# Performance work log

Measured on AMD Instinct MI355X. Metric: run time of the kernel, lower is better.

## Reference

```python
import jax, jax.numpy as jnp
import numpy as np


def setup_inputs() -> dict:
    key = jax.random.key(0)
    k0, k1, k2, k3 = jax.random.split(key, 4)
    T, H, I, E = 2048, 2048, 5632, 8
    return {
        "hidden_states": jax.random.normal(k0, (T, H), dtype=jnp.float32),
        "gate_w": jax.random.normal(k1, (E, H), dtype=jnp.float32) * 0.02,
        "w1": jax.random.normal(k2, (E, 2 * I, H), dtype=jnp.float32) * 0.02,
        "w2": jax.random.normal(k3, (E, H, I), dtype=jnp.float32) * 0.02,
        "top_k": 2,
    }


def reference(hidden_states, gate_w, w1, w2, top_k):
    # hidden_states: [T, H]; gate_w: [E, H]; w1: [E, 2I, H]; w2: [E, H, I]
    T = hidden_states.shape[0]
    E = w1.shape[0]
    router_logits = hidden_states @ gate_w.T                    # [T, E]
    probs = jax.nn.softmax(router_logits, axis=-1)
    topk_w, topk_idx = jax.lax.top_k(probs, top_k)              # [T, k]
    # renormalize=False in fused_moe: use raw softmax top-k weights.
    # Dense combine matrix C[t, e] = weight of expert e for token t (0 if unrouted).
    combine = jnp.zeros((T, E), dtype=probs.dtype)
    combine = combine.at[jnp.arange(T)[:, None], topk_idx].add(topk_w)
    out = jnp.zeros_like(hidden_states)
    for e in range(E):  # small fixed expert loop
        gate_up = hidden_states @ w1[e].T                       # [T, 2I]
        g, u = jnp.split(gate_up, 2, axis=-1)
        h = jax.nn.silu(g) * u                                  # SiluAndMul
        out = out + combine[:, e:e + 1] * (h @ w2[e].T)         # [T, H]
    return out
```

## Files before the change

kernel.cpp:

```cpp
#include <hip/hip_runtime.h>
#include <hip/hip_bf16.h>

typedef __bf16 bf16_t;
typedef __bf16 bf16x4 __attribute__((ext_vector_type(4)));
typedef __bf16 bf16x8 __attribute__((ext_vector_type(8)));
typedef float  f32x4  __attribute__((ext_vector_type(4)));

constexpr int T_ = 2048, H_ = 2048, I_ = 5632, E_ = 8, S_ = T_ * 2;

constexpr size_t OFF_HB    = 0;
constexpr size_t OFF_HOUT  = OFF_HB    + (size_t)T_ * H_ * 2;
constexpr size_t OFF_DPART = OFF_HOUT  + (size_t)S_ * I_ * 2;
constexpr size_t OFF_TOS   = OFF_DPART + (size_t)S_ * H_ * 4;
constexpr size_t OFF_SOT   = OFF_TOS   + (size_t)S_ * 4;
constexpr size_t OFF_TKI   = OFF_SOT   + (size_t)S_ * 4;
constexpr size_t OFF_TKW   = OFF_TKI   + (size_t)S_ * 4;
constexpr size_t OFF_CNT   = OFF_TKW   + (size_t)S_ * 4;
constexpr size_t OFF_OFFS  = OFF_CNT   + 64;
constexpr size_t OFF_CUR   = OFF_OFFS  + 64;

__device__ __forceinline__ void gload16(const void* g, void* l) {
  __builtin_amdgcn_global_load_lds(
      (const __attribute__((address_space(1))) void*)g,
      (__attribute__((address_space(3))) void*)l, 16, 0, 0);
}

__device__ __forceinline__ bf16x4 cvt4(const float4 v) {
  bf16x4 r; r[0]=(bf16_t)v.x; r[1]=(bf16_t)v.y; r[2]=(bf16_t)v.z; r[3]=(bf16_t)v.w;
  return r;
}

__global__ __launch_bounds__(256)
void router_kernel(const float* __restrict__ hs, const float* __restrict__ gw,
                   int* __restrict__ tki, float* __restrict__ tkw,
                   int* __restrict__ counts, bf16_t* __restrict__ hb)
{
  const int t = blockIdx.x;
  const int tid = threadIdx.x;
  const int lane = tid & 63, wid = tid >> 6;
  const float* hrow = hs + (size_t)t * H_;
  const int c0 = tid * 8;
  float4 h0 = *(const float4*)(hrow + c0);
  float4 h1 = *(const float4*)(hrow + c0 + 4);
  bf16x8 hv;
  hv[0]=(bf16_t)h0.x; hv[1]=(bf16_t)h0.y; hv[2]=(bf16_t)h0.z; hv[3]=(bf16_t)h0.w;
  hv[4]=(bf16_t)h1.x; hv[5]=(bf16_t)h1.y; hv[6]=(bf16_t)h1.z; hv[7]=(bf16_t)h1.w;
  *(bf16x8*)(hb + (size_t)t * H_ + c0) = hv;

  float acc[E_];
  #pragma unroll
  for (int e = 0; e < E_; ++e) {
    const float* g = gw + (size_t)e * H_ + c0;
    float4 g0 = *(const float4*)(g);
    float4 g1 = *(const float4*)(g + 4);
    acc[e] = h0.x*g0.x + h0.y*g0.y + h0.z*g0.z + h0.w*g0.w
           + h1.x*g1.x + h1.y*g1.y + h1.z*g1.z + h1.w*g1.w;
  }
  #pragma unroll
  for (int e = 0; e < E_; ++e)
    #pragma unroll
    for (int o = 32; o > 0; o >>= 1)
      acc[e] += __shfl_down(acc[e], o);
  __shared__ float red[4][E_];
  if (lane == 0)
    #pragma unroll
    for (int e = 0; e < E_; ++e) red[wid][e] = acc[e];
  __syncthreads();
  if (tid == 0) {
    float l[E_];
    #pragma unroll
    for (int e = 0; e < E_; ++e) l[e] = red[0][e] + red[1][e] + red[2][e] + red[3][e];
    float m = l[0];
    #pragma unroll
    for (int e = 1; e < E_; ++e) m = fmaxf(m, l[e]);
    float p[E_]; float s = 0.f;
    #pragma unroll
    for (int e = 0; e < E_; ++e) { p[e] = __expf(l[e] - m); s += p[e]; }
    int i1 = 0;
    #pragma unroll
    for (int e = 1; e < E_; ++e) if (l[e] > l[i1]) i1 = e;
    int i2 = (i1 == 0) ? 1 : 0;
    #pragma unroll
    for (int e = 0; e < E_; ++e) if (e != i1 && l[e] > l[i2]) i2 = e;
    tki[2*t] = i1; tki[2*t+1] = i2;
    tkw[2*t] = p[i1] / s; tkw[2*t+1] = p[i2] / s;
    atomicAdd(&counts[i1], 1);
    atomicAdd(&counts[i2], 1);
  }
}

__global__ void scan_kernel(const int* __restrict__ counts, const int* __restrict__ tki,
                            int* __restrict__ offs, int* __restrict__ cursor,
                            int* __restrict__ tos, int* __restrict__ sot)
{
  if (threadIdx.x == 0) {
    int run = 0;
    for (int e = 0; e < E_; ++e) { offs[e] = run; cursor[e] = run; run += counts[e]; }
  }
  __syncthreads();
  for (int t = threadIdx.x; t < T_; t += blockDim.x) {
    #pragma unroll
    for (int k = 0; k < 2; ++k) {
      int e = tki[2*t + k];
      int s = atomicAdd(&cursor[e], 1);
      tos[s] = t;
      sot[2*t + k] = s;
    }
  }
}

constexpr int G1_BM = 128, G1_BN = 64, G1_BK = 64;

__global__ __launch_bounds__(256, 2)
void gemm1_kernel(const bf16_t* __restrict__ hb, const float* __restrict__ w1,
                  const int* __restrict__ tos, const int* __restrict__ offs,
                  const int* __restrict__ counts, bf16_t* __restrict__ hout)
{
  const int bid = blockIdx.x;
  const int e   = bid & 7;
  const int idx = bid >> 3;
  const int mt  = idx & 15;
  const int nt  = idx >> 4;

  const int cnt = counts[e];
  const int m0 = mt * G1_BM;
  if (m0 >= cnt) return;
  const int off = offs[e];
  const int n0 = nt * G1_BN;

  const float* Wg = w1 + (size_t)e * (2 * (size_t)I_ * H_) + (size_t)n0 * H_;
  const float* Wu = Wg + (size_t)I_ * H_;

  __shared__ bf16_t Al [2][G1_BM][G1_BK];
  __shared__ bf16_t Bgl[2][G1_BN][G1_BK];
  __shared__ bf16_t Bul[2][G1_BN][G1_BK];

  const int tid = threadIdx.x;
  const int lane = tid & 63, wid = tid >> 6;
  const int wm = wid >> 1, wn = wid & 1;
  const int l15 = lane & 15, l4 = lane >> 4;

  const bf16_t* agp[4]; int aoff[4];
  #pragma unroll
  for (int i = 0; i < 4; ++i) {
    int q = wid * 4 + i;
    int row = q * 8 + (lane >> 3);
    int slot = off + m0 + row, mx = off + cnt - 1;
    if (slot > mx) slot = mx;
    agp[i]  = hb + (size_t)tos[slot] * H_ + ((lane & 7) ^ (lane >> 3)) * 8;
    aoff[i] = q * 1024;
  }
  const int brow = tid >> 2, bq = tid & 3;
  const float* gsrc = Wg + (size_t)brow * H_;
  const float* usrc = Wu + (size_t)brow * H_;
  int wby[4];
  #pragma unroll
  for (int i = 0; i < 4; ++i)
    wby[i] = brow * 128 + ((8 * bq + 32 * i) ^ ((brow & 7) << 4));

  float4 bgr[4], bur[4];
  auto loadB = [&](int k0) {
    #pragma unroll
    for (int i = 0; i < 4; ++i) bgr[i] = *(const float4*)(gsrc + k0 + 4 * bq + 16 * i);
    #pragma unroll
    for (int i = 0; i < 4; ++i) bur[i] = *(const float4*)(usrc + k0 + 4 * bq + 16 * i);
  };
  auto stageA = [&](int b, int k0) {
    char* base = (char*)&Al[b][0][0];
    #pragma unroll
    for (int i = 0; i < 4; ++i) gload16(agp[i] + k0, base + aoff[i]);
  };
  auto writeB = [&](int b) {
    char* gb = (char*)&Bgl[b][0][0];
    char* ub = (char*)&Bul[b][0][0];
    #pragma unroll
    for (int i = 0; i < 4; ++i) {
      *(bf16x4*)(gb + wby[i]) = cvt4(bgr[i]);
      *(bf16x4*)(ub + wby[i]) = cvt4(bur[i]);
    }
  };

  f32x4 accg[4][2], accu[4][2];
  #pragma unroll
  for (int mi = 0; mi < 4; ++mi)
    #pragma unroll
    for (int ni = 0; ni < 2; ++ni) {
      accg[mi][ni] = f32x4{0.f,0.f,0.f,0.f};
      accu[mi][ni] = f32x4{0.f,0.f,0.f,0.f};
    }

  auto compute = [&](int b) {
    const char* ab = (const char*)&Al[b][0][0];
    const char* gb = (const char*)&Bgl[b][0][0];
    const char* ub = (const char*)&Bul[b][0][0];
    #pragma unroll
    for (int ks = 0; ks < 2; ++ks) {
      const int cb = ks * 64 + l4 * 16;
      bf16x8 af[4], bgf[2], buf2[2];
      #pragma unroll
      for (int mi = 0; mi < 4; ++mi) {
        int r = wm * 64 + mi * 16 + l15;
        af[mi] = *(const bf16x8*)(ab + r * 128 + (cb ^ ((r & 7) << 4)));
      }
      #pragma unroll
      for (int ni = 0; ni < 2; ++ni) {
        int r = wn * 32 + ni * 16 + l15;
        int o = r * 128 + (cb ^ ((r & 7) << 4));
        bgf[ni]  = *(const bf16x8*)(gb + o);
        buf2[ni] = *(const bf16x8*)(ub + o);
      }
      #pragma unroll
      for (int mi = 0; mi < 4; ++mi)
        #pragma unroll
        for (int ni = 0; ni < 2; ++ni) {
          accg[mi][ni] = __builtin_amdgcn_mfma_f32_16x16x32_bf16(af[mi], bgf[ni],  accg[mi][ni], 0, 0, 0);
          accu[mi][ni] = __builtin_amdgcn_mfma_f32_16x16x32_bf16(af[mi], buf2[ni], accu[mi][ni], 0, 0, 0);
        }
    }
  };

  constexpr int NK = H_ / G1_BK;
  stageA(0, 0); loadB(0); writeB(0);
  __syncthreads();
  int cur = 0;
  for (int kt = 0; kt < NK; ++kt) {
    if (kt + 1 < NK) { stageA(cur ^ 1, (kt + 1) * G1_BK); loadB((kt + 1) * G1_BK); }
    compute(cur);
    if (kt + 1 < NK) writeB(cur ^ 1);
    __syncthreads();
    cur ^= 1;
  }

  #pragma unroll
  for (int mi = 0; mi < 4; ++mi)
    #pragma unroll
    for (int ni = 0; ni < 2; ++ni)
      #pragma unroll
      for (int j = 0; j < 4; ++j) {
        int rel = wm*64 + mi*16 + l4*4 + j;
        if (m0 + rel < cnt) {
          int col = n0 + wn*32 + ni*16 + l15;
          float g = accg[mi][ni][j];
          float u = accu[mi][ni][j];
          float hvv = (g / (1.0f + __expf(-g))) * u;
          hout[(size_t)(off + m0 + rel) * I_ + col] = (bf16_t)hvv;
        }
      }
}

constexpr int G2_BM = 128, G2_BN = 128, G2_BK = 64;

__global__ __launch_bounds__(256, 2)
void gemm2_kernel(const bf16_t* __restrict__ hbuf, const float* __restrict__ w2,
                  const int* __restrict__ offs, const int* __restrict__ counts,
                  float* __restrict__ dpart)
{
  const int bid = blockIdx.x;
  const int e   = bid & 7;
  const int idx = bid >> 3;
  const int mt  = idx & 15;
  const int nt  = idx >> 4;

  const int cnt = counts[e];
  const int m0 = mt * G2_BM;
  if (m0 >= cnt) return;
  const int off = offs[e];
  const int n0 = nt * G2_BN;
  const float* W = w2 + (size_t)e * ((size_t)H_ * I_) + (size_t)n0 * I_;

  __shared__ bf16_t Al[2][G2_BM][G2_BK];
  __shared__ bf16_t Bl[2][G2_BN][G2_BK];

  const int tid = threadIdx.x;
  const int lane = tid & 63, wid = tid >> 6;
  const int wm = wid >> 1, wn = wid & 1;
  const int l15 = lane & 15, l4 = lane >> 4;

  const bf16_t* agp[4]; int aoff[4];
  #pragma unroll
  for (int i = 0; i < 4; ++i) {
    int q = wid * 4 + i;
    int row = q * 8 + (lane >> 3);
    int slot = off + m0 + row, mx = off + cnt - 1;
    if (slot > mx) slot = mx;
    agp[i]  = hbuf + (size_t)slot * I_ + ((lane & 7) ^ (lane >> 3)) * 8;
    aoff[i] = q * 1024;
  }
  const int brow = tid >> 1, bq = tid & 1;
  const float* bsrc = W + (size_t)brow * I_;
  int wby[8];
  #pragma unroll
  for (int i = 0; i < 8; ++i)
    wby[i] = brow * 128 + ((8 * bq + 16 * i) ^ ((brow & 7) << 4));

  float4 br[8];
  auto loadB = [&](int k0) {
    #pragma unroll
    for (int i = 0; i < 8; ++i) br[i] = *(const float4*)(bsrc + k0 + 4 * bq + 8 * i);
  };
  auto stageA = [&](int b, int k0) {
    char* base = (char*)&Al[b][0][0];
    #pragma unroll
    for (int i = 0; i < 4; ++i) gload16(agp[i] + k0, base + aoff[i]);
  };
  auto writeB = [&](int b) {
    char* bb = (char*)&Bl[b][0][0];
    #pragma unroll
    for (int i = 0; i < 8; ++i)
      *(bf16x4*)(bb + wby[i]) = cvt4(br[i]);
  };

  f32x4 acc[4][4];
  #pragma unroll
  for (int mi = 0; mi < 4; ++mi)
    #pragma unroll
    for (int ni = 0; ni < 4; ++ni) acc[mi][ni] = f32x4{0.f,0.f,0.f,0.f};

  auto compute = [&](int b) {
    const char* ab = (const char*)&Al[b][0][0];
    const char* bb = (const char*)&Bl[b][0][0];
    #pragma unroll
    for (int ks = 0; ks < 2; ++ks) {
      const int cb = ks * 64 + l4 * 16;
      bf16x8 af[4], bf[4];
      #pragma unroll
      for (int mi = 0; mi < 4; ++mi) {
        int r = wm * 64 + mi * 16 + l15;
        af[mi] = *(const bf16x8*)(ab + r * 128 + (cb ^ ((r & 7) << 4)));
      }
      #pragma unroll
      for (int ni = 0; ni < 4; ++ni) {
        int r = wn * 64 + ni * 16 + l15;
        bf[ni] = *(const bf16x8*)(bb + r * 128 + (cb ^ ((r & 7) << 4)));
      }
      #pragma unroll
      for (int mi = 0; mi < 4; ++mi)
        #pragma unroll
        for (int ni = 0; ni < 4; ++ni)
          acc[mi][ni] = __builtin_amdgcn_mfma_f32_16x16x32_bf16(af[mi], bf[ni], acc[mi][ni], 0, 0, 0);
    }
  };

  constexpr int NK = I_ / G2_BK;
  stageA(0, 0); loadB(0); writeB(0);
  __syncthreads();
  int cur = 0;
  for (int kt = 0; kt < NK; ++kt) {
    if (kt + 1 < NK) { stageA(cur ^ 1, (kt + 1) * G2_BK); loadB((kt + 1) * G2_BK); }
    compute(cur);
    if (kt + 1 < NK) writeB(cur ^ 1);
    __syncthreads();
    cur ^= 1;
  }

  #pragma unroll
  for (int mi = 0; mi < 4; ++mi)
    #pragma unroll
    for (int ni = 0; ni < 4; ++ni)
      #pragma unroll
      for (int j = 0; j < 4; ++j) {
        int rel = wm*64 + mi*16 + l4*4 + j;
        if (m0 + rel < cnt) {
          int col = n0 + wn*64 + ni*16 + l15;
          dpart[(size_t)(off + m0 + rel) * H_ + col] = acc[mi][ni][j];
        }
      }
}

__global__ __launch_bounds__(256)
void combine_kernel(const float* __restrict__ dpart, const int* __restrict__ sot,
                    const float* __restrict__ tkw, float* __restrict__ out)
{
  int idx = blockIdx.x * 256 + threadIdx.x;
  int t = idx >> 9;
  int c = (idx & 511) * 4;
  float wA = tkw[2*t], wB = tkw[2*t+1];
  int sA = sot[2*t], sB = sot[2*t+1];
  float4 a = *(const float4*)(dpart + (size_t)sA * H_ + c);
  float4 b = *(const float4*)(dpart + (size_t)sB * H_ + c);
  float4 o;
  o.x = wA*a.x + wB*b.x; o.y = wA*a.y + wB*b.y;
  o.z = wA*a.z + wB*b.z; o.w = wA*a.w + wB*b.w;
  *(float4*)(out + (size_t)t * H_ + c) = o;
}

extern "C" void kernel_launch(void* const* d_in, const int* in_sizes, int n_in,
                              void* d_out, int out_size, void* d_ws, size_t ws_size,
                              hipStream_t stream) {
  const float* hs = (const float*)d_in[0];
  const float* gw = (const float*)d_in[1];
  const float* w1 = (const float*)d_in[2];
  const float* w2 = (const float*)d_in[3];
  float* out = (float*)d_out;
  char* ws = (char*)d_ws;

  bf16_t* hb    = (bf16_t*)(ws + OFF_HB);
  bf16_t* hout  = (bf16_t*)(ws + OFF_HOUT);
  float*  dpart = (float*) (ws + OFF_DPART);
  int*    tos   = (int*)   (ws + OFF_TOS);
  int*    sot   = (int*)   (ws + OFF_SOT);
  int*    tki   = (int*)   (ws + OFF_TKI);
  float*  tkw   = (float*) (ws + OFF_TKW);
  int*    cnt   = (int*)   (ws + OFF_CNT);
  int*    offp  = (int*)   (ws + OFF_OFFS);
  int*    curp  = (int*)   (ws + OFF_CUR);

  hipMemsetAsync(ws + OFF_CNT, 0, 64, stream);

  router_kernel<<<T_, 256, 0, stream>>>(hs, gw, tki, tkw, cnt, hb);
  scan_kernel<<<1, 256, 0, stream>>>(cnt, tki, offp, curp, tos, sot);
  gemm1_kernel<<<(T_ / G1_BM) * (I_ / G1_BN) * E_, 256, 0, stream>>>(hb, w1, tos, offp, cnt, hout);
  gemm2_kernel<<<(T_ / G2_BM) * (H_ / G2_BN) * E_, 256, 0, stream>>>(hout, w2, offp, cnt, dpart);
  combine_kernel<<<(T_ * H_ / 4) / 256, 256, 0, stream>>>(dpart, sot, tkw, out);
}
```

Measured before the change: 1.033 ms.

## Stage fp32 expert weights directly into LDS via async loads, convert at fragment read

Both expert GEMMs now load the fp32 weight tiles straight into shared memory with global_load_lds, the same way the activations were already loaded. The register staging and the separate bf16 write-back step are gone, and the conversion to bf16 happens when each wave reads its MFMA fragments. This removes register pressure and the in-loop writeB stall, and lets the weight fetch overlap compute asynchronously. To fit the larger fp32 LDS tiles, BK is halved to 32 and the occupancy hint is raised to 3. The barrier also moves to the top of the loop. The trade-offs are redundant conversion across waves, more LDS read bandwidth, and twice as many k-iterations and barriers.

```diff
diff --git a/kernel.cpp b/kernel.cpp
--- a/kernel.cpp
+++ b/kernel.cpp
@@ -2,7 +2,6 @@
 #include <hip/hip_bf16.h>
 
 typedef __bf16 bf16_t;
-typedef __bf16 bf16x4 __attribute__((ext_vector_type(4)));
 typedef __bf16 bf16x8 __attribute__((ext_vector_type(8)));
 typedef float  f32x4  __attribute__((ext_vector_type(4)));
 
@@ -23,11 +22,6 @@
   __builtin_amdgcn_global_load_lds(
       (const __attribute__((address_space(1))) void*)g,
       (__attribute__((address_space(3))) void*)l, 16, 0, 0);
-}
-
-__device__ __forceinline__ bf16x4 cvt4(const float4 v) {
-  bf16x4 r; r[0]=(bf16_t)v.x; r[1]=(bf16_t)v.y; r[2]=(bf16_t)v.z; r[3]=(bf16_t)v.w;
-  return r;
 }
 
 __global__ __launch_bounds__(256)
@@ -109,9 +103,9 @@
   }
 }
 
-constexpr int G1_BM = 128, G1_BN = 64, G1_BK = 64;
-
-__global__ __launch_bounds__(256, 2)
+constexpr int G1_BM = 128, G1_BN = 64, G1_BK = 32;
+
+__global__ __launch_bounds__(256, 3)
 void gemm1_kernel(const bf16_t* __restrict__ hb, const float* __restrict__ w1,
                   const int* __restrict__ tos, const int* __restrict__ offs,
                   const int* __restrict__ counts, bf16_t* __restrict__ hout)
@@ -132,52 +126,45 @@
   const float* Wu = Wg + (size_t)I_ * H_;
 
   __shared__ bf16_t Al [2][G1_BM][G1_BK];
-  __shared__ bf16_t Bgl[2][G1_BN][G1_BK];
-  __shared__ bf16_t Bul[2][G1_BN][G1_BK];
+  __shared__ float  Bgl[2][G1_BN][G1_BK];
+  __shared__ float  Bul[2][G1_BN][G1_BK];
 
   const int tid = threadIdx.x;
   const int lane = tid & 63, wid = tid >> 6;
   const int wm = wid >> 1, wn = wid & 1;
   const int l15 = lane & 15, l4 = lane >> 4;
 
-  const bf16_t* agp[4]; int aoff[4];
-  #pragma unroll
-  for (int i = 0; i < 4; ++i) {
-    int q = wid * 4 + i;
-    int row = q * 8 + (lane >> 3);
+  const bf16_t* agp[2]; int aoff[2];
+  #pragma unroll
+  for (int i = 0; i < 2; ++i) {
+    int q = wid * 2 + i;
+    int row = q * 16 + (lane >> 2);
     int slot = off + m0 + row, mx = off + cnt - 1;
     if (slot > mx) slot = mx;
-    agp[i]  = hb + (size_t)tos[slot] * H_ + ((lane & 7) ^ (lane >> 3)) * 8;
+    agp[i]  = hb + (size_t)tos[slot] * H_ + (lane & 3) * 8;
     aoff[i] = q * 1024;
   }
-  const int brow = tid >> 2, bq = tid & 3;
-  const float* gsrc = Wg + (size_t)brow * H_;
-  const float* usrc = Wu + (size_t)brow * H_;
-  int wby[4];
-  #pragma unroll
-  for (int i = 0; i < 4; ++i)
-    wby[i] = brow * 128 + ((8 * bq + 32 * i) ^ ((brow & 7) << 4));
-
-  float4 bgr[4], bur[4];
-  auto loadB = [&](int k0) {
-    #pragma unroll
-    for (int i = 0; i < 4; ++i) bgr[i] = *(const float4*)(gsrc + k0 + 4 * bq + 16 * i);
-    #pragma unroll
-    for (int i = 0; i < 4; ++i) bur[i] = *(const float4*)(usrc + k0 + 4 * bq + 16 * i);
-  };
-  auto stageA = [&](int b, int k0) {
-    char* base = (char*)&Al[b][0][0];
-    #pragma unroll
-    for (int i = 0; i < 4; ++i) gload16(agp[i] + k0, base + aoff[i]);
-  };
-  auto writeB = [&](int b) {
+  const float* bgp[2]; const float* bup[2]; int boff[2];
+  #pragma unroll
+  for (int i = 0; i < 2; ++i) {
+    int q = wid * 2 + i;
+    int row = q * 8 + (lane >> 3);
+    int scol = ((lane & 7) ^ (lane >> 3)) * 4;
+    bgp[i]  = Wg + (size_t)row * H_ + scol;
+    bup[i]  = Wu + (size_t)row * H_ + scol;
+    boff[i] = q * 1024;
+  }
+
+  auto stage = [&](int b, int k0) {
+    char* ab = (char*)&Al [b][0][0];
     char* gb = (char*)&Bgl[b][0][0];
     char* ub = (char*)&Bul[b][0][0];
     #pragma unroll
-    for (int i = 0; i < 4; ++i) {
-      *(bf16x4*)(gb + wby[i]) = cvt4(bgr[i]);
-      *(bf16x4*)(ub + wby[i]) = cvt4(bur[i]);
-    }
+    for (int i = 0; i < 2; ++i) gload16(agp[i] + k0, ab + aoff[i]);
+    #pragma unroll
+    for (int i = 0; i < 2; ++i) gload16(bgp[i] + k0, gb + boff[i]);
+    #pragma unroll
+    for (int i = 0; i < 2; ++i) gload16(bup[i] + k0, ub + boff[i]);
   };
 
   f32x4 accg[4][2], accu[4][2];
@@ -190,44 +177,50 @@
     }
 
   auto compute = [&](int b) {
-    const char* ab = (const char*)&Al[b][0][0];
+    const char* ab = (const char*)&Al [b][0][0];
     const char* gb = (const char*)&Bgl[b][0][0];
     const char* ub = (const char*)&Bul[b][0][0];
-    #pragma unroll
-    for (int ks = 0; ks < 2; ++ks) {
-      const int cb = ks * 64 + l4 * 16;
-      bf16x8 af[4], bgf[2], buf2[2];
-      #pragma unroll
-      for (int mi = 0; mi < 4; ++mi) {
-        int r = wm * 64 + mi * 16 + l15;
-        af[mi] = *(const bf16x8*)(ab + r * 128 + (cb ^ ((r & 7) << 4)));
+    bf16x8 af[4], bgf[2], buf2[2];
+    #pragma unroll
+    for (int mi = 0; mi < 4; ++mi) {
+      int r = wm * 64 + mi * 16 + l15;
+      af[mi] = *(const bf16x8*)(ab + r * 64 + l4 * 16);
+    }
+    #pragma unroll
+    for (int ni = 0; ni < 2; ++ni) {
+      int r = wn * 32 + ni * 16 + l15;
+      const char* rbg = gb + r * 128;
+      const char* rbu = ub + r * 128;
+      int c0 = (l4 * 32)      ^ ((r & 7) << 4);
+      int c1 = (l4 * 32 + 16) ^ ((r & 7) << 4);
+      f32x4 g0 = *(const f32x4*)(rbg + c0);
+      f32x4 g1 = *(const f32x4*)(rbg + c1);
+      f32x4 u0 = *(const f32x4*)(rbu + c0);
+      f32x4 u1 = *(const f32x4*)(rbu + c1);
+      #pragma unroll
+      for (int j = 0; j < 4; ++j) {
+        bgf[ni][j]     = (bf16_t)g0[j];
+        bgf[ni][j + 4] = (bf16_t)g1[j];
+        buf2[ni][j]     = (bf16_t)u0[j];
+        buf2[ni][j + 4] = (bf16_t)u1[j];
       }
+    }
+    #pragma unroll
+    for (int mi = 0; mi < 4; ++mi)
       #pragma unroll
       for (int ni = 0; ni < 2; ++ni) {
-        int r = wn * 32 + ni * 16 + l15;
-        int o = r * 128 + (cb ^ ((r & 7) << 4));
-        bgf[ni]  = *(const bf16x8*)(gb + o);
-        buf2[ni] = *(const bf16x8*)(ub + o);
+        accg[mi][ni] = __builtin_amdgcn_mfma_f32_16x16x32_bf16(af[mi], bgf[ni],  accg[mi][ni], 0, 0, 0);
+        accu[mi][ni] = __builtin_amdgcn_mfma_f32_16x16x32_bf16(af[mi], buf2[ni], accu[mi][ni], 0, 0, 0);
       }
-      #pragma unroll
-      for (int mi = 0; mi < 4; ++mi)
-        #pragma unroll
-        for (int ni = 0; ni < 2; ++ni) {
-          accg[mi][ni] = __builtin_amdgcn_mfma_f32_16x16x32_bf16(af[mi], bgf[ni],  accg[mi][ni], 0, 0, 0);
-          accu[mi][ni] = __builtin_amdgcn_mfma_f32_16x16x32_bf16(af[mi], buf2[ni], accu[mi][ni], 0, 0, 0);
-        }
-    }
   };
 
   constexpr int NK = H_ / G1_BK;
-  stageA(0, 0); loadB(0); writeB(0);
-  __syncthreads();
+  stage(0, 0);
   int cur = 0;
   for (int kt = 0; kt < NK; ++kt) {
-    if (kt + 1 < NK) { stageA(cur ^ 1, (kt + 1) * G1_BK); loadB((kt + 1) * G1_BK); }
+    __syncthreads();
+    if (kt + 1 < NK) stage(cur ^ 1, (kt + 1) * G1_BK);
     compute(cur);
-    if (kt + 1 < NK) writeB(cur ^ 1);
-    __syncthreads();
     cur ^= 1;
   }
 
@@ -248,9 +241,9 @@
       }
 }
 
-constexpr int G2_BM = 128, G2_BN = 128, G2_BK = 64;
-
-__global__ __launch_bounds__(256, 2)
+constexpr int G2_BM = 128, G2_BN = 128, G2_BK = 32;
+
+__global__ __launch_bounds__(256, 3)
 void gemm2_kernel(const bf16_t* __restrict__ hbuf, const float* __restrict__ w2,
                   const int* __restrict__ offs, const int* __restrict__ counts,
                   float* __restrict__ dpart)
@@ -269,45 +262,40 @@
   const float* W = w2 + (size_t)e * ((size_t)H_ * I_) + (size_t)n0 * I_;
 
   __shared__ bf16_t Al[2][G2_BM][G2_BK];
-  __shared__ bf16_t Bl[2][G2_BN][G2_BK];
+  __shared__ float  Bl[2][G2_BN][G2_BK];
 
   const int tid = threadIdx.x;
   const int lane = tid & 63, wid = tid >> 6;
   const int wm = wid >> 1, wn = wid & 1;
   const int l15 = lane & 15, l4 = lane >> 4;
 
-  const bf16_t* agp[4]; int aoff[4];
+  const bf16_t* agp[2]; int aoff[2];
+  #pragma unroll
+  for (int i = 0; i < 2; ++i) {
+    int q = wid * 2 + i;
+    int row = q * 16 + (lane >> 2);
+    int slot = off + m0 + row, mx = off + cnt - 1;
+    if (slot > mx) slot = mx;
+    agp[i]  = hbuf + (size_t)slot * I_ + (lane & 3) * 8;
+    aoff[i] = q * 1024;
+  }
+  const float* bp[4]; int boff[4];
   #pragma unroll
   for (int i = 0; i < 4; ++i) {
     int q = wid * 4 + i;
     int row = q * 8 + (lane >> 3);
-    int slot = off + m0 + row, mx = off + cnt - 1;
-    if (slot > mx) slot = mx;
-    agp[i]  = hbuf + (size_t)slot * I_ + ((lane & 7) ^ (lane >> 3)) * 8;
-    aoff[i] = q * 1024;
-  }
-  const int brow = tid >> 1, bq = tid & 1;
-  const float* bsrc = W + (size_t)brow * I_;
-  int wby[8];
-  #pragma unroll
-  for (int i = 0; i < 8; ++i)
-    wby[i] = brow * 128 + ((8 * bq + 16 * i) ^ ((brow & 7) << 4));
-
-  float4 br[8];
-  auto loadB = [&](int k0) {
-    #pragma unroll
-    for (int i = 0; i < 8; ++i) br[i] = *(const float4*)(bsrc + k0 + 4 * bq + 8 * i);
-  };
-  auto stageA = [&](int b, int k0) {
-    char* base = (char*)&Al[b][0][0];
-    #pragma unroll
-    for (int i = 0; i < 4; ++i) gload16(agp[i] + k0, base + aoff[i]);
-  };
-  auto writeB = [&](int b) {
+    int scol = ((lane & 7) ^ (lane >> 3)) * 4;
+    bp[i]   = W + (size_t)row * I_ + scol;
+    boff[i] = q * 1024;
+  }
+
+  auto stage = [&](int b, int k0) {
+    char* ab = (char*)&Al[b][0][0];
     char* bb = (char*)&Bl[b][0][0];
     #pragma unroll
-    for (int i = 0; i < 8; ++i)
-      *(bf16x4*)(bb + wby[i]) = cvt4(br[i]);
+    for (int i = 0; i < 2; ++i) gload16(agp[i] + k0, ab + aoff[i]);
+    #pragma unroll
+    for (int i = 0; i < 4; ++i) gload16(bp[i] + k0, bb + boff[i]);
   };
 
   f32x4 acc[4][4];
@@ -319,37 +307,40 @@
   auto compute = [&](int b) {
     const char* ab = (const char*)&Al[b][0][0];
     const char* bb = (const char*)&Bl[b][0][0];
-    #pragma unroll
-    for (int ks = 0; ks < 2; ++ks) {
-      const int cb = ks * 64 + l4 * 16;
-      bf16x8 af[4], bf[4];
-      #pragma unroll
-      for (int mi = 0; mi < 4; ++mi) {
-        int r = wm * 64 + mi * 16 + l15;
-        af[mi] = *(const bf16x8*)(ab + r * 128 + (cb ^ ((r & 7) << 4)));
+    bf16x8 af[4], bf[4];
+    #pragma unroll
+    for (int mi = 0; mi < 4; ++mi) {
+      int r = wm * 64 + mi * 16 + l15;
+      af[mi] = *(const bf16x8*)(ab + r * 64 + l4 * 16);
+    }
+    #pragma unroll
+    for (int ni = 0; ni < 4; ++ni) {
+      int r = wn * 64 + ni * 16 + l15;
+      const char* rb = bb + r * 128;
+      int c0 = (l4 * 32)      ^ ((r & 7) << 4);
+      int c1 = (l4 * 32 + 16) ^ ((r & 7) << 4);
+      f32x4 b0 = *(const f32x4*)(rb + c0);
+      f32x4 b1 = *(const f32x4*)(rb + c1);
+      #pragma unroll
+      for (int j = 0; j < 4; ++j) {
+        bf[ni][j]     = (bf16_t)b0[j];
+        bf[ni][j + 4] = (bf16_t)b1[j];
       }
-      #pragma unroll
-      for (int ni = 0; ni < 4; ++ni) {
-        int r = wn * 64 + ni * 16 + l15;
-        bf[ni] = *(const bf16x8*)(bb + r * 128 + (cb ^ ((r & 7) << 4)));
-      }
-      #pragma unroll
-      for (int mi = 0; mi < 4; ++mi)
-        #pragma unroll
-        for (int ni = 0; ni < 4; ++ni)
-          acc[mi][ni] = __builtin_amdgcn_mfma_f32_16x16x32_bf16(af[mi], bf[ni], acc[mi][ni], 0, 0, 0);
-    }
+    }
+    #pragma unroll
+    for (int mi = 0; mi < 4; ++mi)
+      #pragma unroll
+      for (int ni = 0; ni < 4; ++ni)
+        acc[mi][ni] = __builtin_amdgcn_mfma_f32_16x16x32_bf16(af[mi], bf[ni], acc[mi][ni], 0, 0, 0);
   };
 
   constexpr int NK = I_ / G2_BK;
-  stageA(0, 0); loadB(0); writeB(0);
-  __syncthreads();
+  stage(0, 0);
   int cur = 0;
   for (int kt = 0; kt < NK; ++kt) {
-    if (kt + 1 < NK) { stageA(cur ^ 1, (kt + 1) * G2_BK); loadB((kt + 1) * G2_BK); }
+    __syncthreads();
+    if (kt + 1 < NK) stage(cur ^ 1, (kt + 1) * G2_BK);
     compute(cur);
-    if (kt + 1 < NK) writeB(cur ^ 1);
-    __syncthreads();
     cur ^= 1;
   }
 
```

Measured after the change: 1.420 ms. +37.5%, slower.
